# Kernel optimization log

Hardware: AMD Instinct MI355X
Metric: run time of the kernel (lower is better)

Reference implementation:

```python
import jax, jax.numpy as jnp
import numpy as np

B, S, E, H = 2, 2048, 768, 8
D = E // H  # 96
SCALING = D ** (-0.5)


def setup_inputs() -> dict:
    key = jax.random.key(0)
    ks = jax.random.split(key, 7)
    sd = E ** -0.5
    return {
        "x": jax.random.normal(ks[0], (B, S, E), jnp.float32),
        "Wq": jax.random.normal(ks[1], (E, E), jnp.float32) * sd,
        "bq": jax.random.normal(ks[2], (E,), jnp.float32) * 0.02,
        "Wk": jax.random.normal(ks[3], (E, E), jnp.float32) * sd,
        "bk": jax.random.normal(ks[4], (E,), jnp.float32) * 0.02,
        "Wo": jax.random.normal(ks[5], (E, E), jnp.float32) * sd,
        "bo": jax.random.normal(ks[6], (E,), jnp.float32) * 0.02,
    }


def _split_heads(t):
    # [B, S, E] -> [B, H, S, D]
    return t.reshape(B, S, H, D).transpose(0, 2, 1, 3)


def reference(x, Wq, bq, Wk, bk, Wo, bo):
    q = _split_heads(x @ Wq + bq)
    k = _split_heads(x @ Wk + bk)
    # NOTE: faithful to source bug — values use the KEY projection
    v = _split_heads(x @ Wk + bk)
    energies = jnp.einsum("bhqd,bhkd->bhqk", q, k)  # [B,H,S,S]
    # NOTE: faithful to source — scaling applied AFTER softmax
    attn = jax.nn.softmax(energies, axis=-1) * SCALING
    out = jnp.einsum("bhqk,bhkd->bhqd", attn, v)
    out = out.transpose(0, 2, 1, 3).reshape(B, S, E)
    return out @ Wo + bo
```

## Files before the change

### kernel.cpp

```cpp
#include <hip/hip_runtime.h>
#include <hip/hip_bf16.h>
#include <math.h>
#include <stdint.h>

#define B_DIM 2
#define S_DIM 2048
#define E_DIM 768
#define H_DIM 8
#define D_DIM 96
#define M_DIM (B_DIM*S_DIM)
#define SCALE_F 0.10206207261596575f

typedef _Float16 f16x8 __attribute__((ext_vector_type(8)));
typedef float    f32x4  __attribute__((ext_vector_type(4)));
typedef float    f32x16 __attribute__((ext_vector_type(16)));

#define MFMA16H(a,b,c) __builtin_amdgcn_mfma_f32_16x16x32_f16(a,b,c,0,0,0)
#define MFMA32H(a,b,c) __builtin_amdgcn_mfma_f32_32x32x16_f16(a,b,c,0,0,0)

__device__ inline unsigned short f2h(float f) {
    return __builtin_bit_cast(unsigned short, (_Float16)f);
}

__device__ inline void gload16(const void* g, void* l) {
    auto gp = reinterpret_cast<const __attribute__((address_space(1))) uint32_t*>(
        reinterpret_cast<uintptr_t>(g));
    auto lp = reinterpret_cast<__attribute__((address_space(3))) uint32_t*>(
        reinterpret_cast<uintptr_t>(l));
    __builtin_amdgcn_global_load_lds(gp, lp, 16, 0, 0);
}

__global__ __launch_bounds__(256) void convert_x_kernel(
    const float* __restrict__ X, unsigned short* __restrict__ Xf)
{
    int i = (blockIdx.x * 256 + threadIdx.x) * 4;
    float4 v = *(const float4*)(X + i);
    ushort4 h;
    h.x = f2h(v.x); h.y = f2h(v.y); h.z = f2h(v.z); h.w = f2h(v.w);
    *(ushort4*)(Xf + i) = h;
}

__global__ __launch_bounds__(256) void convert_wT3_kernel(
    const float* __restrict__ W0, const float* __restrict__ W1,
    const float* __restrict__ W2,
    unsigned short* __restrict__ T0, unsigned short* __restrict__ T1,
    unsigned short* __restrict__ T2)
{
    const float* W; unsigned short* T;
    if (blockIdx.z == 0)      { W = W0; T = T0; }
    else if (blockIdx.z == 1) { W = W1; T = T1; }
    else                      { W = W2; T = T2; }

    __shared__ float tile[64][65];
    const int tid = threadIdx.x;
    const int k0 = blockIdx.y << 6, n0 = blockIdx.x << 6;
    const int r = tid >> 4, c4 = (tid & 15) << 2;
    #pragma unroll
    for (int i = 0; i < 4; ++i) {
        float4 v = *(const float4*)(W + (size_t)(k0 + r + i*16)*E_DIM + n0 + c4);
        tile[r + i*16][c4+0] = v.x; tile[r + i*16][c4+1] = v.y;
        tile[r + i*16][c4+2] = v.z; tile[r + i*16][c4+3] = v.w;
    }
    __syncthreads();
    #pragma unroll
    for (int i = 0; i < 4; ++i) {
        int n = r + i*16;
        ushort4 h;
        h.x = f2h(tile[c4+0][n]); h.y = f2h(tile[c4+1][n]);
        h.z = f2h(tile[c4+2][n]); h.w = f2h(tile[c4+3][n]);
        *(ushort4*)(T + (size_t)(n0 + n)*E_DIM + k0 + c4) = h;
    }
}

__global__ __launch_bounds__(256) void gemm_qk_kernel(
    const unsigned short* __restrict__ A, const unsigned short* __restrict__ Bt,
    const float* __restrict__ bq, const float* __restrict__ bk,
    unsigned short* __restrict__ Qf, unsigned short* __restrict__ Kf)
{
    __shared__ unsigned short sA[128*32];
    __shared__ unsigned short sB[128*32];

    const int tid  = threadIdx.x;
    const int lane = tid & 63;
    const int w    = tid >> 6;
    const int qn   = lane & 15, quad = lane >> 4;
    const int wm   = w & 1, wn = w >> 1;
    const int row0 = blockIdx.y << 7;
    const int col0 = blockIdx.x << 7;

    const int sr = tid >> 2;
    const int sk = (tid & 3) << 3;

    const unsigned short* gA = A  + (size_t)(row0 + sr)*E_DIM + sk;
    const unsigned short* gB = Bt + (size_t)(col0 + sr)*E_DIM + sk;

    f32x4 acc[4][4];
    #pragma unroll
    for (int mt = 0; mt < 4; ++mt)
        #pragma unroll
        for (int nt = 0; nt < 4; ++nt)
            { acc[mt][nt][0]=0.f; acc[mt][nt][1]=0.f; acc[mt][nt][2]=0.f; acc[mt][nt][3]=0.f; }

    for (int k0 = 0; k0 < E_DIM; k0 += 32) {
        __syncthreads();
        gload16(gA + k0,            sA + tid*8);
        gload16(gA + 64*E_DIM + k0, sA + 2048 + tid*8);
        gload16(gB + k0,            sB + tid*8);
        gload16(gB + 64*E_DIM + k0, sB + 2048 + tid*8);
        __syncthreads();

        f16x8 af[4], bf[4];
        #pragma unroll
        for (int mt = 0; mt < 4; ++mt)
            af[mt] = *(const f16x8*)&sA[(wm*64 + mt*16 + qn)*32 + quad*8];
        #pragma unroll
        for (int nt = 0; nt < 4; ++nt)
            bf[nt] = *(const f16x8*)&sB[(wn*64 + nt*16 + qn)*32 + quad*8];
        #pragma unroll
        for (int mt = 0; mt < 4; ++mt)
            #pragma unroll
            for (int nt = 0; nt < 4; ++nt)
                acc[mt][nt] = MFMA16H(af[mt], bf[nt], acc[mt][nt]);
    }

    #pragma unroll
    for (int nt = 0; nt < 4; ++nt) {
        int n = col0 + wn*64 + nt*16 + qn;
        bool isQ = n < E_DIM;
        float bias = isQ ? bq[n] : bk[n - E_DIM];
        unsigned short* op = isQ ? Qf : Kf;
        int nc = isQ ? n : n - E_DIM;
        #pragma unroll
        for (int mt = 0; mt < 4; ++mt)
            #pragma unroll
            for (int r = 0; r < 4; ++r) {
                int m = row0 + wm*64 + mt*16 + quad*4 + r;
                op[(size_t)m*E_DIM + nc] = f2h(acc[mt][nt][r] + bias);
            }
    }
}

__global__ __launch_bounds__(256) void gemm_out_kernel(
    const unsigned short* __restrict__ A, const unsigned short* __restrict__ Bt,
    const float* __restrict__ bo, float* __restrict__ out)
{
    __shared__ unsigned short sA[128*32];
    __shared__ unsigned short sB[64*32];

    const int tid  = threadIdx.x;
    const int lane = tid & 63;
    const int w    = tid >> 6;
    const int qn   = lane & 15, quad = lane >> 4;
    const int wm   = w & 1, wn = w >> 1;
    const int row0 = blockIdx.y << 7;
    const int col0 = blockIdx.x << 6;

    const int sr = tid >> 2;
    const int sk = (tid & 3) << 3;

    const unsigned short* gA = A  + (size_t)(row0 + sr)*E_DIM + sk;
    const unsigned short* gB = Bt + (size_t)(col0 + sr)*E_DIM + sk;

    f32x4 acc[4][2];
    #pragma unroll
    for (int mt = 0; mt < 4; ++mt)
        #pragma unroll
        for (int nt = 0; nt < 2; ++nt)
            { acc[mt][nt][0]=0.f; acc[mt][nt][1]=0.f; acc[mt][nt][2]=0.f; acc[mt][nt][3]=0.f; }

    for (int k0 = 0; k0 < E_DIM; k0 += 32) {
        __syncthreads();
        gload16(gA + k0,            sA + tid*8);
        gload16(gA + 64*E_DIM + k0, sA + 2048 + tid*8);
        gload16(gB + k0,            sB + tid*8);
        __syncthreads();

        f16x8 af[4], bf[2];
        #pragma unroll
        for (int mt = 0; mt < 4; ++mt)
            af[mt] = *(const f16x8*)&sA[(wm*64 + mt*16 + qn)*32 + quad*8];
        #pragma unroll
        for (int nt = 0; nt < 2; ++nt)
            bf[nt] = *(const f16x8*)&sB[(wn*32 + nt*16 + qn)*32 + quad*8];
        #pragma unroll
        for (int mt = 0; mt < 4; ++mt)
            #pragma unroll
            for (int nt = 0; nt < 2; ++nt)
                acc[mt][nt] = MFMA16H(af[mt], bf[nt], acc[mt][nt]);
    }

    #pragma unroll
    for (int nt = 0; nt < 2; ++nt) {
        int n = col0 + wn*32 + nt*16 + qn;
        float bias = bo[n];
        #pragma unroll
        for (int mt = 0; mt < 4; ++mt)
            #pragma unroll
            for (int r = 0; r < 4; ++r) {
                int m = row0 + wm*64 + mt*16 + quad*4 + r;
                out[(size_t)m*E_DIM + n] = acc[mt][nt][r] + bias;
            }
    }
}

__global__ __launch_bounds__(256) void attn_mfma_kernel(
    const unsigned short* __restrict__ Qf, const unsigned short* __restrict__ Kf,
    unsigned short* __restrict__ O0, unsigned short* __restrict__ O1,
    float2* __restrict__ ml)
{
    __shared__ unsigned short sKh[64][104];
    __shared__ unsigned short sKt[96][72];
    __shared__ unsigned short sPs[128][72];

    const int tid  = threadIdx.x;
    const int w    = tid >> 6;
    const int lane = tid & 63;
    const int col  = lane & 31;
    const int half = lane >> 5;
    const int b    = blockIdx.z >> 1;
    const int kh   = blockIdx.z & 1;
    const int h    = blockIdx.y;
    const int q0   = blockIdx.x << 7;
    const int key0 = kh << 10;

    f16x8 qf[6];
    {
        const size_t ro = ((size_t)(b*S_DIM + q0 + w*32 + col))*E_DIM
                          + h*D_DIM + half*8;
        #pragma unroll
        for (int kc = 0; kc < 6; ++kc)
            qf[kc] = *(const f16x8*)(Qf + ro + kc*16);
    }

    f32x16 o[3];
    #pragma unroll
    for (int nt = 0; nt < 3; ++nt)
        #pragma unroll
        for (int r = 0; r < 16; ++r) o[nt][r] = 0.f;
    float m_i = -INFINITY, l_i = 0.f;

    const bool stager = tid < 128;
    const int st = tid & 127;
    const int sp = st >> 2;
    const int dq = st & 3;

    uint4 r0[3], r1[3];
    if (stager) {
        const size_t g0 = ((size_t)(b*S_DIM + key0 + 2*sp))*E_DIM + h*D_DIM + dq*24;
        #pragma unroll
        for (int i = 0; i < 3; ++i) {
            r0[i] = *(const uint4*)(Kf + g0 + 8*i);
            r1[i] = *(const uint4*)(Kf + g0 + E_DIM + 8*i);
        }
    }

    for (int kt = 0; kt < 16; ++kt) {
        __syncthreads();
        if (stager) {
            #pragma unroll
            for (int i = 0; i < 3; ++i) {
                *(uint4*)&sKh[2*sp  ][dq*24 + 8*i] = r0[i];
                *(uint4*)&sKh[2*sp+1][dq*24 + 8*i] = r1[i];
            }
            const unsigned short* p0 = (const unsigned short*)r0;
            const unsigned short* p1 = (const unsigned short*)r1;
            #pragma unroll
            for (int c = 0; c < 24; ++c) {
                unsigned int pk = (unsigned int)p0[c] | ((unsigned int)p1[c] << 16);
                *(unsigned int*)&sKt[dq*24 + c][2*sp] = pk;
            }
        }
        __syncthreads();

        if (stager && kt + 1 < 16) {
            const size_t g0 = ((size_t)(b*S_DIM + key0 + (kt+1)*64 + 2*sp))*E_DIM
                              + h*D_DIM + dq*24;
            #pragma unroll
            for (int i = 0; i < 3; ++i) {
                r0[i] = *(const uint4*)(Kf + g0 + 8*i);
                r1[i] = *(const uint4*)(Kf + g0 + E_DIM + 8*i);
            }
        }

        f32x16 s[2];
        #pragma unroll
        for (int mt = 0; mt < 2; ++mt) {
            f32x16 acc;
            #pragma unroll
            for (int r = 0; r < 16; ++r) acc[r] = 0.f;
            #pragma unroll
            for (int kc = 0; kc < 6; ++kc) {
                f16x8 ah = *(const f16x8*)&sKh[mt*32 + col][kc*16 + half*8];
                acc = MFMA32H(ah, qf[kc], acc);
            }
            s[mt] = acc;
        }

        float mx = s[0][0];
        #pragma unroll
        for (int mt = 0; mt < 2; ++mt)
            #pragma unroll
            for (int r = 0; r < 16; ++r) mx = fmaxf(mx, s[mt][r]);
        mx = fmaxf(mx, __shfl_xor(mx, 32));

        float m_new = fmaxf(m_i, mx);
        float alpha = __expf(m_i - m_new);
        m_i = m_new;

        float psum = 0.f;
        #pragma unroll
        for (int mt = 0; mt < 2; ++mt)
            #pragma unroll
            for (int g = 0; g < 4; ++g) {
                float e0 = __expf(s[mt][4*g+0] - m_new);
                float e1 = __expf(s[mt][4*g+1] - m_new);
                float e2 = __expf(s[mt][4*g+2] - m_new);
                float e3 = __expf(s[mt][4*g+3] - m_new);
                psum += e0 + e1 + e2 + e3;
                ushort4 pk;
                pk.x = f2h(e0); pk.y = f2h(e1); pk.z = f2h(e2); pk.w = f2h(e3);
                *(ushort4*)&sPs[w*32 + col][mt*32 + 8*g + 4*half] = pk;
            }
        psum += __shfl_xor(psum, 32);
        l_i = l_i * alpha + psum;

        #pragma unroll
        for (int g = 0; g < 4; ++g)
            #pragma unroll
            for (int r = 0; r < 4; ++r) {
                float ar = __shfl(alpha, 8*g + r + 4*half);
                #pragma unroll
                for (int nt = 0; nt < 3; ++nt) o[nt][4*g + r] *= ar;
            }

        #pragma unroll
        for (int kc = 0; kc < 4; ++kc) {
            f16x8 pa = *(const f16x8*)&sPs[w*32 + col][kc*16 + half*8];
            #pragma unroll
            for (int nt = 0; nt < 3; ++nt) {
                f16x8 vb = *(const f16x8*)&sKt[nt*32 + col][kc*16 + half*8];
                o[nt] = MFMA32H(pa, vb, o[nt]);
            }
        }
    }

    unsigned short* Ob = (kh ? O1 : O0)
        + ((size_t)(b*S_DIM + q0 + w*32))*E_DIM + h*D_DIM;
    #pragma unroll
    for (int g = 0; g < 4; ++g)
        #pragma unroll
        for (int r = 0; r < 4; ++r) {
            int qr = 8*g + r + 4*half;
            #pragma unroll
            for (int nt = 0; nt < 3; ++nt)
                Ob[(size_t)qr*E_DIM + nt*32 + col] = f2h(o[nt][4*g + r]);
        }
    if (lane < 32) {
        int q = q0 + w*32 + lane;
        ml[((size_t)(kh*B_DIM + b)*H_DIM + h)*S_DIM + q] = make_float2(m_i, l_i);
    }
}

__global__ __launch_bounds__(256) void combine_kernel(
    const unsigned short* __restrict__ O0, const unsigned short* __restrict__ O1,
    const float2* __restrict__ ml, unsigned short* __restrict__ ctx)
{
    size_t idx = ((size_t)blockIdx.x * 256 + threadIdx.x) * 4;
    int row = (int)(idx / E_DIM);
    int ce  = (int)(idx % E_DIM);
    int h   = ce / D_DIM;
    int b   = row >> 11;
    int q   = row & (S_DIM - 1);

    float2 m0 = ml[((size_t)(0*B_DIM + b)*H_DIM + h)*S_DIM + q];
    float2 m1 = ml[((size_t)(1*B_DIM + b)*H_DIM + h)*S_DIM + q];
    float m  = fmaxf(m0.x, m1.x);
    float w0 = __expf(m0.x - m), w1 = __expf(m1.x - m);
    float l  = m0.y * w0 + m1.y * w1;
    float s0 = w0 * SCALE_F / l, s1 = w1 * SCALE_F / l;

    ushort4 a = *(const ushort4*)(O0 + idx);
    ushort4 c = *(const ushort4*)(O1 + idx);
    ushort4 o;
    o.x = f2h((float)__builtin_bit_cast(_Float16, a.x)*s0 + (float)__builtin_bit_cast(_Float16, c.x)*s1);
    o.y = f2h((float)__builtin_bit_cast(_Float16, a.y)*s0 + (float)__builtin_bit_cast(_Float16, c.y)*s1);
    o.z = f2h((float)__builtin_bit_cast(_Float16, a.z)*s0 + (float)__builtin_bit_cast(_Float16, c.z)*s1);
    o.w = f2h((float)__builtin_bit_cast(_Float16, a.w)*s0 + (float)__builtin_bit_cast(_Float16, c.w)*s1);
    *(ushort4*)(ctx + idx) = o;
}

extern "C" void kernel_launch(void* const* d_in, const int* in_sizes, int n_in,
                              void* d_out, int out_size, void* d_ws, size_t ws_size,
                              hipStream_t stream)
{
    const float* x  = (const float*)d_in[0];
    const float* Wq = (const float*)d_in[1];
    const float* bq = (const float*)d_in[2];
    const float* Wk = (const float*)d_in[3];
    const float* bk = (const float*)d_in[4];
    const float* Wo = (const float*)d_in[5];
    const float* bo = (const float*)d_in[6];
    float* out = (float*)d_out;

    const size_t NE = (size_t)M_DIM * E_DIM;
    const size_t WE = (size_t)E_DIM * E_DIM;
    unsigned short* xf   = (unsigned short*)d_ws;
    unsigned short* WqkT = xf + NE;
    unsigned short* WoT  = WqkT + 2*WE;
    unsigned short* Qf   = WoT + WE;
    unsigned short* Kf   = Qf + NE;
    unsigned short* ctx  = Kf + NE;
    float2*         mlbuf = (float2*)(ctx + NE);
    unsigned short* Oh0  = xf;
    unsigned short* Oh1  = (unsigned short*)d_out;

    dim3 blk(256);
    hipLaunchKernelGGL(convert_x_kernel, dim3(NE/1024), blk, 0, stream, x, xf);
    hipLaunchKernelGGL(convert_wT3_kernel, dim3(12,12,3), blk, 0, stream,
                       Wq, Wk, Wo, WqkT, WqkT + WE, WoT);

    hipLaunchKernelGGL(gemm_qk_kernel, dim3(12,32), blk, 0, stream,
                       xf, WqkT, bq, bk, Qf, Kf);

    hipLaunchKernelGGL(attn_mfma_kernel, dim3(S_DIM/128, H_DIM, B_DIM*2), blk, 0,
                       stream, Qf, Kf, Oh0, Oh1, mlbuf);

    hipLaunchKernelGGL(combine_kernel, dim3(NE/1024), blk, 0, stream,
                       Oh0, Oh1, mlbuf, ctx);

    hipLaunchKernelGGL(gemm_out_kernel, dim3(12,32), blk, 0, stream,
                       ctx, WoT, bo, out);
}
```

Before: 168.3 us.

## Fuse input conversion and split combine into GEMMs, use three-way key split

The fp32-to-fp16 conversion of x moves into the QK projection GEMM, which loads float4 from global memory, converts in registers and prefetches the next tile. The attention split-K goes from two to three key chunks, and the softmax switches to exp2 with log2e folded into Q. The attention kernel also transposes its MFMA operands so the rescale by alpha needs no shuffles. The combine kernel is replaced by a small per-row scale kernel, and the weighted sum of the three partial outputs is done while staging the A tile of the output GEMM. Both GEMMs use 64-row tiles to launch more blocks, at the cost of less reuse per block and an extra partial-output buffer to read.

Measured after the change: 196.4 us. 16.7% more time.

```diff
diff --git a/kernel.cpp b/kernel.cpp
--- a/kernel.cpp
+++ b/kernel.cpp
@@ -10,6 +10,7 @@
 #define D_DIM 96
 #define M_DIM (B_DIM*S_DIM)
 #define SCALE_F 0.10206207261596575f
+#define LOG2E_F 1.4426950408889634f
 
 typedef _Float16 f16x8 __attribute__((ext_vector_type(8)));
 typedef float    f32x4  __attribute__((ext_vector_type(4)));
@@ -20,6 +21,9 @@
 
 __device__ inline unsigned short f2h(float f) {
     return __builtin_bit_cast(unsigned short, (_Float16)f);
+}
+__device__ inline float h2f(unsigned short u) {
+    return (float)__builtin_bit_cast(_Float16, u);
 }
 
 __device__ inline void gload16(const void* g, void* l) {
@@ -30,16 +34,6 @@
     __builtin_amdgcn_global_load_lds(gp, lp, 16, 0, 0);
 }
 
-__global__ __launch_bounds__(256) void convert_x_kernel(
-    const float* __restrict__ X, unsigned short* __restrict__ Xf)
-{
-    int i = (blockIdx.x * 256 + threadIdx.x) * 4;
-    float4 v = *(const float4*)(X + i);
-    ushort4 h;
-    h.x = f2h(v.x); h.y = f2h(v.y); h.z = f2h(v.z); h.w = f2h(v.w);
-    *(ushort4*)(Xf + i) = h;
-}
-
 __global__ __launch_bounds__(256) void convert_wT3_kernel(
     const float* __restrict__ W0, const float* __restrict__ W1,
     const float* __restrict__ W2,
@@ -73,11 +67,11 @@
 }
 
 __global__ __launch_bounds__(256) void gemm_qk_kernel(
-    const unsigned short* __restrict__ A, const unsigned short* __restrict__ Bt,
+    const float* __restrict__ X, const unsigned short* __restrict__ Bt,
     const float* __restrict__ bq, const float* __restrict__ bk,
     unsigned short* __restrict__ Qf, unsigned short* __restrict__ Kf)
 {
-    __shared__ unsigned short sA[128*32];
+    __shared__ unsigned short sA[64*32];
     __shared__ unsigned short sB[128*32];
 
     const int tid  = threadIdx.x;
@@ -85,39 +79,51 @@
     const int w    = tid >> 6;
     const int qn   = lane & 15, quad = lane >> 4;
     const int wm   = w & 1, wn = w >> 1;
-    const int row0 = blockIdx.y << 7;
+    const int row0 = blockIdx.y << 6;
     const int col0 = blockIdx.x << 7;
 
-    const int sr = tid >> 2;
-    const int sk = (tid & 3) << 3;
-
-    const unsigned short* gA = A  + (size_t)(row0 + sr)*E_DIM + sk;
-    const unsigned short* gB = Bt + (size_t)(col0 + sr)*E_DIM + sk;
-
-    f32x4 acc[4][4];
-    #pragma unroll
-    for (int mt = 0; mt < 4; ++mt)
+    const int ar = tid >> 2;
+    const int ak = (tid & 3) << 3;
+    const float* gA = X + (size_t)(row0 + ar)*E_DIM + ak;
+    const unsigned short* gB = Bt + (size_t)(col0 + ar)*E_DIM + ak;
+
+    f32x4 acc[2][4];
+    #pragma unroll
+    for (int mt = 0; mt < 2; ++mt)
         #pragma unroll
         for (int nt = 0; nt < 4; ++nt)
             { acc[mt][nt][0]=0.f; acc[mt][nt][1]=0.f; acc[mt][nt][2]=0.f; acc[mt][nt][3]=0.f; }
 
+    float4 a0 = *(const float4*)(gA);
+    float4 a1 = *(const float4*)(gA + 4);
+
     for (int k0 = 0; k0 < E_DIM; k0 += 32) {
         __syncthreads();
-        gload16(gA + k0,            sA + tid*8);
-        gload16(gA + 64*E_DIM + k0, sA + 2048 + tid*8);
-        gload16(gB + k0,            sB + tid*8);
-        gload16(gB + 64*E_DIM + k0, sB + 2048 + tid*8);
-        __syncthreads();
-
-        f16x8 af[4], bf[4];
-        #pragma unroll
-        for (int mt = 0; mt < 4; ++mt)
-            af[mt] = *(const f16x8*)&sA[(wm*64 + mt*16 + qn)*32 + quad*8];
+        {
+            ushort4 h0, h1;
+            h0.x = f2h(a0.x); h0.y = f2h(a0.y); h0.z = f2h(a0.z); h0.w = f2h(a0.w);
+            h1.x = f2h(a1.x); h1.y = f2h(a1.y); h1.z = f2h(a1.z); h1.w = f2h(a1.w);
+            *(ushort4*)&sA[tid*8]     = h0;
+            *(ushort4*)&sA[tid*8 + 4] = h1;
+        }
+        gload16(gB + k0,              sB + tid*8);
+        gload16(gB + 64*E_DIM + k0,   sB + 2048 + tid*8);
+        __syncthreads();
+
+        if (k0 + 32 < E_DIM) {
+            a0 = *(const float4*)(gA + k0 + 32);
+            a1 = *(const float4*)(gA + k0 + 36);
+        }
+
+        f16x8 af[2], bf[4];
+        #pragma unroll
+        for (int mt = 0; mt < 2; ++mt)
+            af[mt] = *(const f16x8*)&sA[(wm*32 + mt*16 + qn)*32 + quad*8];
         #pragma unroll
         for (int nt = 0; nt < 4; ++nt)
             bf[nt] = *(const f16x8*)&sB[(wn*64 + nt*16 + qn)*32 + quad*8];
         #pragma unroll
-        for (int mt = 0; mt < 4; ++mt)
+        for (int mt = 0; mt < 2; ++mt)
             #pragma unroll
             for (int nt = 0; nt < 4; ++nt)
                 acc[mt][nt] = MFMA16H(af[mt], bf[nt], acc[mt][nt]);
@@ -128,23 +134,199 @@
         int n = col0 + wn*64 + nt*16 + qn;
         bool isQ = n < E_DIM;
         float bias = isQ ? bq[n] : bk[n - E_DIM];
+        float post = isQ ? LOG2E_F : 1.0f;
         unsigned short* op = isQ ? Qf : Kf;
         int nc = isQ ? n : n - E_DIM;
         #pragma unroll
-        for (int mt = 0; mt < 4; ++mt)
+        for (int mt = 0; mt < 2; ++mt)
             #pragma unroll
             for (int r = 0; r < 4; ++r) {
-                int m = row0 + wm*64 + mt*16 + quad*4 + r;
-                op[(size_t)m*E_DIM + nc] = f2h(acc[mt][nt][r] + bias);
-            }
-    }
+                int m = row0 + wm*32 + mt*16 + quad*4 + r;
+                op[(size_t)m*E_DIM + nc] = f2h((acc[mt][nt][r] + bias) * post);
+            }
+    }
+}
+
+__global__ __launch_bounds__(256) void attn_mfma_kernel(
+    const unsigned short* __restrict__ Qf, const unsigned short* __restrict__ Kf,
+    unsigned short* __restrict__ O0, unsigned short* __restrict__ O1,
+    unsigned short* __restrict__ O2, float2* __restrict__ ml)
+{
+    __shared__ unsigned short sKh[64][98];
+    __shared__ unsigned short sKt[96][66];
+    __shared__ unsigned short sPs[128][66];
+
+    const int tid  = threadIdx.x;
+    const int w    = tid >> 6;
+    const int lane = tid & 63;
+    const int col  = lane & 31;
+    const int half = lane >> 5;
+    const int z    = blockIdx.z;
+    const int b    = z / 3;
+    const int kv   = z % 3;
+    const int h    = blockIdx.y;
+    const int q0   = blockIdx.x << 7;
+    const int key0 = kv * 704;
+    const int ktiles = (kv < 2) ? 11 : 10;
+
+    f16x8 qf[6];
+    {
+        const size_t ro = ((size_t)(b*S_DIM + q0 + w*32 + col))*E_DIM
+                          + h*D_DIM + half*8;
+        #pragma unroll
+        for (int kc = 0; kc < 6; ++kc)
+            qf[kc] = *(const f16x8*)(Qf + ro + kc*16);
+    }
+
+    f32x16 o[3];
+    #pragma unroll
+    for (int nt = 0; nt < 3; ++nt)
+        #pragma unroll
+        for (int r = 0; r < 16; ++r) o[nt][r] = 0.f;
+    float m_i = -INFINITY, l_i = 0.f;
+
+    const bool stager = tid < 128;
+    const int st = tid & 127;
+    const int sp = st >> 2;
+    const int dq = st & 3;
+
+    uint4 r0[3], r1[3];
+    if (stager) {
+        const size_t g0 = ((size_t)(b*S_DIM + key0 + 2*sp))*E_DIM + h*D_DIM + dq*24;
+        #pragma unroll
+        for (int i = 0; i < 3; ++i) {
+            r0[i] = *(const uint4*)(Kf + g0 + 8*i);
+            r1[i] = *(const uint4*)(Kf + g0 + E_DIM + 8*i);
+        }
+    }
+
+    for (int kt = 0; kt < ktiles; ++kt) {
+        __syncthreads();
+        if (stager) {
+            #pragma unroll
+            for (int i = 0; i < 3; ++i) {
+                *(uint4*)&sKh[2*sp  ][dq*24 + 8*i] = r0[i];
+                *(uint4*)&sKh[2*sp+1][dq*24 + 8*i] = r1[i];
+            }
+            const unsigned short* p0 = (const unsigned short*)r0;
+            const unsigned short* p1 = (const unsigned short*)r1;
+            #pragma unroll
+            for (int c = 0; c < 24; ++c) {
+                unsigned int pk = (unsigned int)p0[c] | ((unsigned int)p1[c] << 16);
+                *(unsigned int*)&sKt[dq*24 + c][2*sp] = pk;
+            }
+        }
+        __syncthreads();
+
+        if (stager && kt + 1 < ktiles) {
+            const size_t g0 = ((size_t)(b*S_DIM + key0 + (kt+1)*64 + 2*sp))*E_DIM
+                              + h*D_DIM + dq*24;
+            #pragma unroll
+            for (int i = 0; i < 3; ++i) {
+                r0[i] = *(const uint4*)(Kf + g0 + 8*i);
+                r1[i] = *(const uint4*)(Kf + g0 + E_DIM + 8*i);
+            }
+        }
+
+        f32x16 s[2];
+        #pragma unroll
+        for (int mt = 0; mt < 2; ++mt) {
+            f32x16 acc;
+            #pragma unroll
+            for (int r = 0; r < 16; ++r) acc[r] = 0.f;
+            #pragma unroll
+            for (int kc = 0; kc < 6; ++kc) {
+                f16x8 ah = *(const f16x8*)&sKh[mt*32 + col][kc*16 + half*8];
+                acc = MFMA32H(ah, qf[kc], acc);
+            }
+            s[mt] = acc;
+        }
+
+        float mx = s[0][0];
+        #pragma unroll
+        for (int mt = 0; mt < 2; ++mt)
+            #pragma unroll
+            for (int r = 0; r < 16; ++r) mx = fmaxf(mx, s[mt][r]);
+        mx = fmaxf(mx, __shfl_xor(mx, 32));
+
+        float m_new = fmaxf(m_i, mx);
+        float alpha = exp2f(m_i - m_new);
+        m_i = m_new;
+
+        float psum = 0.f;
+        #pragma unroll
+        for (int mt = 0; mt < 2; ++mt)
+            #pragma unroll
+            for (int g = 0; g < 4; ++g) {
+                float e0 = exp2f(s[mt][4*g+0] - m_new);
+                float e1 = exp2f(s[mt][4*g+1] - m_new);
+                float e2 = exp2f(s[mt][4*g+2] - m_new);
+                float e3 = exp2f(s[mt][4*g+3] - m_new);
+                psum += e0 + e1 + e2 + e3;
+                ushort4 pk;
+                pk.x = f2h(e0); pk.y = f2h(e1); pk.z = f2h(e2); pk.w = f2h(e3);
+                *(ushort4*)&sPs[w*32 + col][mt*32 + 8*g + 4*half] = pk;
+            }
+        psum += __shfl_xor(psum, 32);
+        l_i = l_i * alpha + psum;
+
+        #pragma unroll
+        for (int nt = 0; nt < 3; ++nt)
+            #pragma unroll
+            for (int r = 0; r < 16; ++r) o[nt][r] *= alpha;
+
+        #pragma unroll
+        for (int kc = 0; kc < 4; ++kc) {
+            f16x8 pb = *(const f16x8*)&sPs[w*32 + col][kc*16 + half*8];
+            #pragma unroll
+            for (int nt = 0; nt < 3; ++nt) {
+                f16x8 va = *(const f16x8*)&sKt[nt*32 + col][kc*16 + half*8];
+                o[nt] = MFMA32H(va, pb, o[nt]);
+            }
+        }
+    }
+
+    unsigned short* Ob = (kv == 0 ? O0 : kv == 1 ? O1 : O2)
+        + ((size_t)(b*S_DIM + q0 + w*32 + col))*E_DIM + h*D_DIM;
+    #pragma unroll
+    for (int nt = 0; nt < 3; ++nt)
+        #pragma unroll
+        for (int rg = 0; rg < 4; ++rg) {
+            ushort4 pk;
+            pk.x = f2h(o[nt][4*rg+0]); pk.y = f2h(o[nt][4*rg+1]);
+            pk.z = f2h(o[nt][4*rg+2]); pk.w = f2h(o[nt][4*rg+3]);
+            *(ushort4*)(Ob + nt*32 + 8*rg + 4*half) = pk;
+        }
+    if (lane < 32) {
+        int q = q0 + w*32 + lane;
+        ml[((size_t)(kv*B_DIM + b)*H_DIM + h)*S_DIM + q] = make_float2(m_i, l_i);
+    }
+}
+
+__global__ __launch_bounds__(256) void scale_kernel(
+    const float2* __restrict__ ml, float4* __restrict__ sc)
+{
+    int idx = blockIdx.x * 256 + threadIdx.x;
+    int m = idx >> 3, h = idx & 7;
+    int b = m >> 11, q = m & (S_DIM - 1);
+    float2 e0 = ml[((size_t)(0*B_DIM + b)*H_DIM + h)*S_DIM + q];
+    float2 e1 = ml[((size_t)(1*B_DIM + b)*H_DIM + h)*S_DIM + q];
+    float2 e2 = ml[((size_t)(2*B_DIM + b)*H_DIM + h)*S_DIM + q];
+    float mm = fmaxf(fmaxf(e0.x, e1.x), e2.x);
+    float w0 = exp2f(e0.x - mm), w1 = exp2f(e1.x - mm), w2 = exp2f(e2.x - mm);
+    float l = e0.y*w0 + e1.y*w1 + e2.y*w2;
+    float inv = SCALE_F / l;
+    float4 s; s.x = w0*inv; s.y = w1*inv; s.z = w2*inv; s.w = 0.f;
+    sc[idx] = s;
 }
 
 __global__ __launch_bounds__(256) void gemm_out_kernel(
-    const unsigned short* __restrict__ A, const unsigned short* __restrict__ Bt,
-    const float* __restrict__ bo, float* __restrict__ out)
-{
-    __shared__ unsigned short sA[128*32];
+    const unsigned short* __restrict__ O0, const unsigned short* __restrict__ O1,
+    const unsigned short* __restrict__ O2, const float4* __restrict__ sc,
+    const unsigned short* __restrict__ Bt, const float* __restrict__ bo,
+    float* __restrict__ out)
+{
+    __shared__ unsigned short sA[64*32];
     __shared__ unsigned short sB[64*32];
 
     const int tid  = threadIdx.x;
@@ -152,38 +334,67 @@
     const int w    = tid >> 6;
     const int qn   = lane & 15, quad = lane >> 4;
     const int wm   = w & 1, wn = w >> 1;
-    const int row0 = blockIdx.y << 7;
+    const int row0 = blockIdx.y << 6;
     const int col0 = blockIdx.x << 6;
 
-    const int sr = tid >> 2;
-    const int sk = (tid & 3) << 3;
-
-    const unsigned short* gA = A  + (size_t)(row0 + sr)*E_DIM + sk;
-    const unsigned short* gB = Bt + (size_t)(col0 + sr)*E_DIM + sk;
-
-    f32x4 acc[4][2];
-    #pragma unroll
-    for (int mt = 0; mt < 4; ++mt)
+    const int ar = tid >> 2;
+    const int ak = (tid & 3) << 3;
+    const size_t arow = (size_t)(row0 + ar)*E_DIM;
+    const unsigned short* gB = Bt + (size_t)(col0 + ar)*E_DIM + ak;
+
+    f32x4 acc[2][2];
+    #pragma unroll
+    for (int mt = 0; mt < 2; ++mt)
         #pragma unroll
         for (int nt = 0; nt < 2; ++nt)
             { acc[mt][nt][0]=0.f; acc[mt][nt][1]=0.f; acc[mt][nt][2]=0.f; acc[mt][nt][3]=0.f; }
 
+    ushort4 u0 = *(const ushort4*)(O0 + arow + ak);
+    ushort4 u1 = *(const ushort4*)(O0 + arow + ak + 4);
+    ushort4 v0 = *(const ushort4*)(O1 + arow + ak);
+    ushort4 v1 = *(const ushort4*)(O1 + arow + ak + 4);
+    ushort4 t0 = *(const ushort4*)(O2 + arow + ak);
+    ushort4 t1 = *(const ushort4*)(O2 + arow + ak + 4);
+    float4  s4 = sc[(size_t)(row0 + ar)*H_DIM + 0];
+
     for (int k0 = 0; k0 < E_DIM; k0 += 32) {
         __syncthreads();
-        gload16(gA + k0,            sA + tid*8);
-        gload16(gA + 64*E_DIM + k0, sA + 2048 + tid*8);
-        gload16(gB + k0,            sB + tid*8);
-        __syncthreads();
-
-        f16x8 af[4], bf[2];
-        #pragma unroll
-        for (int mt = 0; mt < 4; ++mt)
-            af[mt] = *(const f16x8*)&sA[(wm*64 + mt*16 + qn)*32 + quad*8];
+        {
+            ushort4 h0, h1;
+            h0.x = f2h(h2f(u0.x)*s4.x + h2f(v0.x)*s4.y + h2f(t0.x)*s4.z);
+            h0.y = f2h(h2f(u0.y)*s4.x + h2f(v0.y)*s4.y + h2f(t0.y)*s4.z);
+            h0.z = f2h(h2f(u0.z)*s4.x + h2f(v0.z)*s4.y + h2f(t0.z)*s4.z);
+            h0.w = f2h(h2f(u0.w)*s4.x + h2f(v0.w)*s4.y + h2f(t0.w)*s4.z);
+            h1.x = f2h(h2f(u1.x)*s4.x + h2f(v1.x)*s4.y + h2f(t1.x)*s4.z);
+            h1.y = f2h(h2f(u1.y)*s4.x + h2f(v1.y)*s4.y + h2f(t1.y)*s4.z);
+            h1.z = f2h(h2f(u1.z)*s4.x + h2f(v1.z)*s4.y + h2f(t1.z)*s4.z);
+            h1.w = f2h(h2f(u1.w)*s4.x + h2f(v1.w)*s4.y + h2f(t1.w)*s4.z);
+            *(ushort4*)&sA[tid*8]     = h0;
+            *(ushort4*)&sA[tid*8 + 4] = h1;
+        }
+        gload16(gB + k0, sB + tid*8);
+        __syncthreads();
+
+        if (k0 + 32 < E_DIM) {
+            int kn = k0 + 32;
+            u0 = *(const ushort4*)(O0 + arow + kn + ak);
+            u1 = *(const ushort4*)(O0 + arow + kn + ak + 4);
+            v0 = *(const ushort4*)(O1 + arow + kn + ak);
+            v1 = *(const ushort4*)(O1 + arow + kn + ak + 4);
+            t0 = *(const ushort4*)(O2 + arow + kn + ak);
+            t1 = *(const ushort4*)(O2 + arow + kn + ak + 4);
+            s4 = sc[(size_t)(row0 + ar)*H_DIM + kn/D_DIM];
+        }
+
+        f16x8 af[2], bf[2];
+        #pragma unroll
+        for (int mt = 0; mt < 2; ++mt)
+            af[mt] = *(const f16x8*)&sA[(wm*32 + mt*16 + qn)*32 + quad*8];
         #pragma unroll
         for (int nt = 0; nt < 2; ++nt)
             bf[nt] = *(const f16x8*)&sB[(wn*32 + nt*16 + qn)*32 + quad*8];
         #pragma unroll
-        for (int mt = 0; mt < 4; ++mt)
+        for (int mt = 0; mt < 2; ++mt)
             #pragma unroll
             for (int nt = 0; nt < 2; ++nt)
                 acc[mt][nt] = MFMA16H(af[mt], bf[nt], acc[mt][nt]);
@@ -194,199 +405,13 @@
         int n = col0 + wn*32 + nt*16 + qn;
         float bias = bo[n];
         #pragma unroll
-        for (int mt = 0; mt < 4; ++mt)
+        for (int mt = 0; mt < 2; ++mt)
             #pragma unroll
             for (int r = 0; r < 4; ++r) {
-                int m = row0 + wm*64 + mt*16 + quad*4 + r;
+                int m = row0 + wm*32 + mt*16 + quad*4 + r;
                 out[(size_t)m*E_DIM + n] = acc[mt][nt][r] + bias;
             }
     }
-}
-
-__global__ __launch_bounds__(256) void attn_mfma_kernel(
-    const unsigned short* __restrict__ Qf, const unsigned short* __restrict__ Kf,
-    unsigned short* __restrict__ O0, unsigned short* __restrict__ O1,
-    float2* __restrict__ ml)
-{
-    __shared__ unsigned short sKh[64][104];
-    __shared__ unsigned short sKt[96][72];
-    __shared__ unsigned short sPs[128][72];
-
-    const int tid  = threadIdx.x;
-    const int w    = tid >> 6;
-    const int lane = tid & 63;
-    const int col  = lane & 31;
-    const int half = lane >> 5;
-    const int b    = blockIdx.z >> 1;
-    const int kh   = blockIdx.z & 1;
-    const int h    = blockIdx.y;
-    const int q0   = blockIdx.x << 7;
-    const int key0 = kh << 10;
-
-    f16x8 qf[6];
-    {
-        const size_t ro = ((size_t)(b*S_DIM + q0 + w*32 + col))*E_DIM
-                          + h*D_DIM + half*8;
-        #pragma unroll
-        for (int kc = 0; kc < 6; ++kc)
-            qf[kc] = *(const f16x8*)(Qf + ro + kc*16);
-    }
-
-    f32x16 o[3];
-    #pragma unroll
-    for (int nt = 0; nt < 3; ++nt)
-        #pragma unroll
-        for (int r = 0; r < 16; ++r) o[nt][r] = 0.f;
-    float m_i = -INFINITY, l_i = 0.f;
-
-    const bool stager = tid < 128;
-    const int st = tid & 127;
-    const int sp = st >> 2;
-    const int dq = st & 3;
-
-    uint4 r0[3], r1[3];
-    if (stager) {
-        const size_t g0 = ((size_t)(b*S_DIM + key0 + 2*sp))*E_DIM + h*D_DIM + dq*24;
-        #pragma unroll
-        for (int i = 0; i < 3; ++i) {
-            r0[i] = *(const uint4*)(Kf + g0 + 8*i);
-            r1[i] = *(const uint4*)(Kf + g0 + E_DIM + 8*i);
-        }
-    }
-
-    for (int kt = 0; kt < 16; ++kt) {
-        __syncthreads();
-        if (stager) {
-            #pragma unroll
-            for (int i = 0; i < 3; ++i) {
-                *(uint4*)&sKh[2*sp  ][dq*24 + 8*i] = r0[i];
-                *(uint4*)&sKh[2*sp+1][dq*24 + 8*i] = r1[i];
-            }
-            const unsigned short* p0 = (const unsigned short*)r0;
-            const unsigned short* p1 = (const unsigned short*)r1;
-            #pragma unroll
-            for (int c = 0; c < 24; ++c) {
-                unsigned int pk = (unsigned int)p0[c] | ((unsigned int)p1[c] << 16);
-                *(unsigned int*)&sKt[dq*24 + c][2*sp] = pk;
-            }
-        }
-        __syncthreads();
-
-        if (stager && kt + 1 < 16) {
-            const size_t g0 = ((size_t)(b*S_DIM + key0 + (kt+1)*64 + 2*sp))*E_DIM
-                              + h*D_DIM + dq*24;
-            #pragma unroll
-            for (int i = 0; i < 3; ++i) {
-                r0[i] = *(const uint4*)(Kf + g0 + 8*i);
-                r1[i] = *(const uint4*)(Kf + g0 + E_DIM + 8*i);
-            }
-        }
-
-        f32x16 s[2];
-        #pragma unroll
-        for (int mt = 0; mt < 2; ++mt) {
-            f32x16 acc;
-            #pragma unroll
-            for (int r = 0; r < 16; ++r) acc[r] = 0.f;
-            #pragma unroll
-            for (int kc = 0; kc < 6; ++kc) {
-                f16x8 ah = *(const f16x8*)&sKh[mt*32 + col][kc*16 + half*8];
-                acc = MFMA32H(ah, qf[kc], acc);
-            }
-            s[mt] = acc;
-        }
-
-        float mx = s[0][0];
-        #pragma unroll
-        for (int mt = 0; mt < 2; ++mt)
-            #pragma unroll
-            for (int r = 0; r < 16; ++r) mx = fmaxf(mx, s[mt][r]);
-        mx = fmaxf(mx, __shfl_xor(mx, 32));
-
-        float m_new = fmaxf(m_i, mx);
-        float alpha = __expf(m_i - m_new);
-        m_i = m_new;
-
-        float psum = 0.f;
-        #pragma unroll
-        for (int mt = 0; mt < 2; ++mt)
-            #pragma unroll
-            for (int g = 0; g < 4; ++g) {
-                float e0 = __expf(s[mt][4*g+0] - m_new);
-                float e1 = __expf(s[mt][4*g+1] - m_new);
-                float e2 = __expf(s[mt][4*g+2] - m_new);
-                float e3 = __expf(s[mt][4*g+3] - m_new);
-                psum += e0 + e1 + e2 + e3;
-                ushort4 pk;
-                pk.x = f2h(e0); pk.y = f2h(e1); pk.z = f2h(e2); pk.w = f2h(e3);
-                *(ushort4*)&sPs[w*32 + col][mt*32 + 8*g + 4*half] = pk;
-            }
-        psum += __shfl_xor(psum, 32);
-        l_i = l_i * alpha + psum;
-
-        #pragma unroll
-        for (int g = 0; g < 4; ++g)
-            #pragma unroll
-            for (int r = 0; r < 4; ++r) {
-                float ar = __shfl(alpha, 8*g + r + 4*half);
-                #pragma unroll
-                for (int nt = 0; nt < 3; ++nt) o[nt][4*g + r] *= ar;
-            }
-
-        #pragma unroll
-        for (int kc = 0; kc < 4; ++kc) {
-            f16x8 pa = *(const f16x8*)&sPs[w*32 + col][kc*16 + half*8];
-            #pragma unroll
-            for (int nt = 0; nt < 3; ++nt) {
-                f16x8 vb = *(const f16x8*)&sKt[nt*32 + col][kc*16 + half*8];
-                o[nt] = MFMA32H(pa, vb, o[nt]);
-            }
-        }
-    }
-
-    unsigned short* Ob = (kh ? O1 : O0)
-        + ((size_t)(b*S_DIM + q0 + w*32))*E_DIM + h*D_DIM;
-    #pragma unroll
-    for (int g = 0; g < 4; ++g)
-        #pragma unroll
-        for (int r = 0; r < 4; ++r) {
-            int qr = 8*g + r + 4*half;
-            #pragma unroll
-            for (int nt = 0; nt < 3; ++nt)
-                Ob[(size_t)qr*E_DIM + nt*32 + col] = f2h(o[nt][4*g + r]);
-        }
-    if (lane < 32) {
-        int q = q0 + w*32 + lane;
-        ml[((size_t)(kh*B_DIM + b)*H_DIM + h)*S_DIM + q] = make_float2(m_i, l_i);
-    }
-}
-
-__global__ __launch_bounds__(256) void combine_kernel(
-    const unsigned short* __restrict__ O0, const unsigned short* __restrict__ O1,
-    const float2* __restrict__ ml, unsigned short* __restrict__ ctx)
-{
-    size_t idx = ((size_t)blockIdx.x * 256 + threadIdx.x) * 4;
-    int row = (int)(idx / E_DIM);
-    int ce  = (int)(idx % E_DIM);
-    int h   = ce / D_DIM;
-    int b   = row >> 11;
-    int q   = row & (S_DIM - 1);
-
-    float2 m0 = ml[((size_t)(0*B_DIM + b)*H_DIM + h)*S_DIM + q];
-    float2 m1 = ml[((size_t)(1*B_DIM + b)*H_DIM + h)*S_DIM + q];
-    float m  = fmaxf(m0.x, m1.x);
-    float w0 = __expf(m0.x - m), w1 = __expf(m1.x - m);
-    float l  = m0.y * w0 + m1.y * w1;
-    float s0 = w0 * SCALE_F / l, s1 = w1 * SCALE_F / l;
-
-    ushort4 a = *(const ushort4*)(O0 + idx);
-    ushort4 c = *(const ushort4*)(O1 + idx);
-    ushort4 o;
-    o.x = f2h((float)__builtin_bit_cast(_Float16, a.x)*s0 + (float)__builtin_bit_cast(_Float16, c.x)*s1);
-    o.y = f2h((float)__builtin_bit_cast(_Float16, a.y)*s0 + (float)__builtin_bit_cast(_Float16, c.y)*s1);
-    o.z = f2h((float)__builtin_bit_cast(_Float16, a.z)*s0 + (float)__builtin_bit_cast(_Float16, c.z)*s1);
-    o.w = f2h((float)__builtin_bit_cast(_Float16, a.w)*s0 + (float)__builtin_bit_cast(_Float16, c.w)*s1);
-    *(ushort4*)(ctx + idx) = o;
 }
 
 extern "C" void kernel_launch(void* const* d_in, const int* in_sizes, int n_in,
@@ -404,30 +429,29 @@
 
     const size_t NE = (size_t)M_DIM * E_DIM;
     const size_t WE = (size_t)E_DIM * E_DIM;
-    unsigned short* xf   = (unsigned short*)d_ws;
-    unsigned short* WqkT = xf + NE;
+    unsigned short* WqkT = (unsigned short*)d_ws;
     unsigned short* WoT  = WqkT + 2*WE;
     unsigned short* Qf   = WoT + WE;
     unsigned short* Kf   = Qf + NE;
-    unsigned short* ctx  = Kf + NE;
-    float2*         mlbuf = (float2*)(ctx + NE);
-    unsigned short* Oh0  = xf;
-    unsigned short* Oh1  = (unsigned short*)d_out;
+    unsigned short* Oh0  = Kf + NE;
+    unsigned short* Oh1  = Oh0 + NE;
+    unsigned short* Oh2  = Oh1 + NE;
+    float2*         mlbuf = (float2*)(Oh2 + NE);
+    float4*         scbuf = (float4*)(mlbuf + 3*(size_t)B_DIM*H_DIM*S_DIM);
 
     dim3 blk(256);
-    hipLaunchKernelGGL(convert_x_kernel, dim3(NE/1024), blk, 0, stream, x, xf);
     hipLaunchKernelGGL(convert_wT3_kernel, dim3(12,12,3), blk, 0, stream,
                        Wq, Wk, Wo, WqkT, WqkT + WE, WoT);
 
-    hipLaunchKernelGGL(gemm_qk_kernel, dim3(12,32), blk, 0, stream,
-                       xf, WqkT, bq, bk, Qf, Kf);
-
-    hipLaunchKernelGGL(attn_mfma_kernel, dim3(S_DIM/128, H_DIM, B_DIM*2), blk, 0,
-                       stream, Qf, Kf, Oh0, Oh1, mlbuf);
-
-    hipLaunchKernelGGL(combine_kernel, dim3(NE/1024), blk, 0, stream,
-                       Oh0, Oh1, mlbuf, ctx);
-
-    hipLaunchKernelGGL(gemm_out_kernel, dim3(12,32), blk, 0, stream,
-                       ctx, WoT, bo, out);
-}
+    hipLaunchKernelGGL(gemm_qk_kernel, dim3(12,64), blk, 0, stream,
+                       x, WqkT, bq, bk, Qf, Kf);
+
+    hipLaunchKernelGGL(attn_mfma_kernel, dim3(S_DIM/128, H_DIM, B_DIM*3), blk, 0,
+                       stream, Qf, Kf, Oh0, Oh1, Oh2, mlbuf);
+
+    hipLaunchKernelGGL(scale_kernel, dim3(M_DIM*H_DIM/256), blk, 0, stream,
+                       mlbuf, scbuf);
+
+    hipLaunchKernelGGL(gemm_out_kernel, dim3(12,64), blk, 0, stream,
+                       Oh0, Oh1, Oh2, scbuf, WoT, bo, out);
+}
```
